# Optimization experiments

Measured on AMD Instinct MI355X. Metric: run time of the kernel, lower is better.

The kernel has to match this reference:

```python
import jax, jax.numpy as jnp
import numpy as np

T = 262144
S_IN, A_IN, S_OUT, G_OUT, H = 64, 16, 32, 16, 32


def setup_inputs() -> dict:
    key = jax.random.key(0)
    ks = jax.random.split(key, 16)
    def lin_w(k, i, o):
        return (jax.random.normal(k, (i, o), jnp.float32) / np.sqrt(i)).astype(jnp.float32)
    return {
        's': jax.random.normal(ks[0], (1, T, S_IN), jnp.float32),
        'a': jax.random.uniform(ks[1], (1, T, A_IN), jnp.float32),  # BCE targets in [0,1]
        'u': jax.random.uniform(ks[2], (1, T, 1), jnp.float32),     # Bernoulli noise
        'W1': lin_w(ks[3], 2 * (S_IN + A_IN), H), 'b1': jnp.zeros((H,), jnp.float32),
        'W2': lin_w(ks[4], 2 * H, H),             'b2': jnp.zeros((H,), jnp.float32),
        'W3': lin_w(ks[5], 2 * H, S_OUT + G_OUT + 1), 'b3': jnp.zeros((S_OUT + G_OUT + 1,), jnp.float32),
        'Wp1': lin_w(ks[6], S_IN + G_OUT, H),     'bp1': jnp.zeros((H,), jnp.float32),
        'Wp2': lin_w(ks[7], H, A_IN),             'bp2': jnp.zeros((A_IN,), jnp.float32),
    }


def gnn_layer(x, W, b):
    # GraphNetLayer: each node sees its own feature + global mean over the trajectory
    agg = jnp.broadcast_to(jnp.mean(x, axis=1, keepdims=True), x.shape)
    return jnp.concatenate([x, agg], axis=-1) @ W + b


def reference(s, a, u, W1, b1, W2, b2, W3, b3, Wp1, bp1, Wp2, bp2):
    # encode: GNN over [N,T,s_in+a_in]
    x = jnp.concatenate([s, a], axis=-1)
    h = jnp.tanh(gnn_layer(x, W1, b1))
    h = jnp.tanh(gnn_layer(h, W2, b2))
    out = gnn_layer(h, W3, b3)
    z, g, alpha_logit = jnp.split(out, [S_OUT, S_OUT + G_OUT], axis=-1)
    alpha = jax.nn.sigmoid(alpha_logit)

    # Bernoulli sample with externalized noise; no gradient through the sample
    hard_alpha = jax.lax.stop_gradient((u < alpha).astype(alpha.dtype))  # [1,T,1]
    log_probs = hard_alpha * jax.nn.log_sigmoid(alpha_logit) + (1.0 - hard_alpha) * jax.nn.log_sigmoid(-alpha_logit)
    reinforce_lp = jnp.mean(log_probs)

    # extend_goals_hard: carry last goal where alpha fired (N==1), ragged scan
    def step(prev, ga):
        gt, at = ga  # [G_OUT], [1]
        cur = jnp.where(at > 0, gt, prev)
        return cur, cur
    _, hard_g = jax.lax.scan(step, jnp.zeros((G_OUT,), g.dtype), (g[0], hard_alpha[0]))
    hard_g = hard_g[None]  # [1,T,G_OUT]

    # decode: goal-conditioned policy MLP
    logits = jnp.tanh(jnp.concatenate([s, hard_g], axis=-1) @ Wp1 + bp1) @ Wp2 + bp2

    # BCEWithLogits recon loss (use_prior=False, train_dynamics/correspondence=False)
    recon = -(a * jax.nn.log_sigmoid(logits) + (1.0 - a) * jax.nn.log_sigmoid(-logits))
    per_ts = recon
    loss = jnp.mean(per_ts) + reinforce_lp * jnp.mean(jax.lax.stop_gradient(per_ts))

    # padded equivalents of short_z/short_g (ragged gather z[0,mask]) returned as masked tensors
    return loss, logits, hard_alpha, hard_g
```

## Files before the change

### kernel.cpp

```cpp
#include <hip/hip_runtime.h>
#include <math.h>


#define TT 262144
#define NBT 1024
#define NBR 512

__device__ __forceinline__ float spf32(float x) {
  return fmaxf(x, 0.f) + log1pf(expf(-fabsf(x)));
}

__device__ __forceinline__ double exp64(double x) {
  const double LOG2E  = 1.4426950408889634074;
  const double LN2_HI = 6.93147180369123816490e-01;
  const double LN2_LO = 1.90821492927058770002e-10;
  double kd = rint(x * LOG2E);
  double r  = fma(-kd, LN2_HI, x);
  r = fma(-kd, LN2_LO, r);
  double p = 2.08767569878681e-9;
  p = fma(p, r, 2.505210838544172e-8);
  p = fma(p, r, 2.755731922398589e-7);
  p = fma(p, r, 2.7557319223985893e-6);
  p = fma(p, r, 2.48015873015873e-5);
  p = fma(p, r, 1.984126984126984e-4);
  p = fma(p, r, 1.388888888888889e-3);
  p = fma(p, r, 8.333333333333333e-3);
  p = fma(p, r, 4.1666666666666664e-2);
  p = fma(p, r, 1.6666666666666666e-1);
  p = fma(p, r, 0.5);
  p = fma(p, r, 1.0);
  p = fma(p, r, 1.0);
  int k = (int)kd;
  long long sb = ((long long)(k + 1023)) << 52;
  return p * __longlong_as_double(sb);
}

__device__ __forceinline__ double tanh64(double x) {
  double ax = fmin(fabs(x), 19.0);
  double e = exp64(2.0 * ax);
  double t = 1.0 - 2.0 / (e + 1.0);
  return x >= 0.0 ? t : -t;
}

template <int C>
__global__ __launch_bounds__(256) void reduce_cols(const float* __restrict__ in,
                                                   double* __restrict__ part) {
  const int rpb = 256 / C;
  int col = threadIdx.x & (C - 1);
  int sub = threadIdx.x / C;
  long row0 = (long)blockIdx.x * rpb + sub;
  long stride = (long)NBR * rpb;
  double acc = 0.0;
  for (long r = row0; r < TT; r += stride) acc += (double)in[r * C + col];
  __shared__ double sm[256];
  sm[threadIdx.x] = acc;
  __syncthreads();
  if (threadIdx.x < C) {
    double s = 0.0;
#pragma unroll
    for (int i = 0; i < rpb; ++i) s += sm[i * C + threadIdx.x];
    part[(long)blockIdx.x * C + threadIdx.x] = s;
  }
}

__global__ __launch_bounds__(640) void prep1(const double* __restrict__ ps_s,
                                             const double* __restrict__ ps_a,
                                             const float* __restrict__ W1,
                                             const float* __restrict__ b1,
                                             double invT, double* __restrict__ c1) {
  __shared__ double partial[80][8];
  __shared__ double mx[80];
  int tid = threadIdx.x;
  int col = tid >> 3, sub = tid & 7;
  double ssum = 0.0;
  if (col < 64) {
#pragma unroll
    for (int i = 0; i < 64; ++i) ssum += ps_s[(sub * 64 + i) * 64 + col];
  } else {
    int c = col - 64;
#pragma unroll
    for (int i = 0; i < 64; ++i) ssum += ps_a[(sub * 64 + i) * 16 + c];
  }
  partial[col][sub] = ssum;
  __syncthreads();
  if (tid < 80) {
    double s = 0.0;
#pragma unroll
    for (int i = 0; i < 8; ++i) s += partial[tid][i];
    mx[tid] = s * invT;
  }
  __syncthreads();
  if (tid < 32) {
    double acc = (double)b1[tid];
    for (int j = 0; j < 80; ++j) acc += mx[j] * (double)W1[(80 + j) * 32 + tid];
    c1[tid] = acc;
  }
}

__global__ __launch_bounds__(256) void prep2(const double* __restrict__ ps,
                                             const float* __restrict__ W2,
                                             const float* __restrict__ b2,
                                             double invT, double* __restrict__ c2) {
  __shared__ double partial[32][8];
  __shared__ double mh[32];
  int tid = threadIdx.x;
  int col = tid >> 3, sub = tid & 7;
  double ssum = 0.0;
#pragma unroll
  for (int i = 0; i < 128; ++i) ssum += ps[(sub * 128 + i) * 32 + col];
  partial[col][sub] = ssum;
  __syncthreads();
  if (tid < 32) {
    double s = 0.0;
#pragma unroll
    for (int i = 0; i < 8; ++i) s += partial[tid][i];
    mh[tid] = s * invT;
  }
  __syncthreads();
  if (tid < 32) {
    double acc = (double)b2[tid];
    for (int j = 0; j < 32; ++j) acc += mh[j] * (double)W2[(32 + j) * 32 + tid];
    c2[tid] = acc;
  }
}

__global__ __launch_bounds__(256) void prep3(const double* __restrict__ ps,
                                             const float* __restrict__ W3,
                                             const float* __restrict__ b3,
                                             double invT, double* __restrict__ c3) {
  __shared__ double partial[32][8];
  __shared__ double mh[32];
  int tid = threadIdx.x;
  int col = tid >> 3, sub = tid & 7;
  double ssum = 0.0;
#pragma unroll
  for (int i = 0; i < 128; ++i) ssum += ps[(sub * 128 + i) * 32 + col];
  partial[col][sub] = ssum;
  __syncthreads();
  if (tid < 32) {
    double s = 0.0;
#pragma unroll
    for (int i = 0; i < 8; ++i) s += partial[tid][i];
    mh[tid] = s * invT;
  }
  __syncthreads();
  if (tid < 17) {
    double acc = (double)b3[32 + tid];
    for (int j = 0; j < 32; ++j) acc += mh[j] * (double)W3[(32 + j) * 49 + 32 + tid];
    c3[tid] = acc;
  }
}


__global__ __launch_bounds__(256, 4) void h1_kernel(const float* __restrict__ s,
                                                    const float* __restrict__ a,
                                                    const float* __restrict__ W1,
                                                    const double* __restrict__ c1,
                                                    double* __restrict__ h,
                                                    double* __restrict__ ps_h) {
  __shared__ float Wl[80 * 32];
  __shared__ double ws[4 * 32];
  for (int i = threadIdx.x; i < 80 * 32; i += 256) Wl[i] = W1[i];
  __syncthreads();
  long t = (long)blockIdx.x * 256 + threadIdx.x;
  double acc[32];
#pragma unroll
  for (int k = 0; k < 32; ++k) acc[k] = c1[k];
  const float4* s4 = (const float4*)(s + t * 64);
#pragma unroll 2
  for (int q = 0; q < 16; ++q) {
    float4 v = s4[q];
    const float* w = &Wl[(q * 4) * 32];
    double x0 = (double)v.x, x1 = (double)v.y, x2 = (double)v.z, x3 = (double)v.w;
#pragma unroll
    for (int k = 0; k < 32; ++k)
      acc[k] += x0 * (double)w[k] + x1 * (double)w[32 + k] +
                x2 * (double)w[64 + k] + x3 * (double)w[96 + k];
  }
  const float4* a4 = (const float4*)(a + t * 16);
#pragma unroll 2
  for (int q = 0; q < 4; ++q) {
    float4 v = a4[q];
    const float* w = &Wl[(64 + q * 4) * 32];
    double x0 = (double)v.x, x1 = (double)v.y, x2 = (double)v.z, x3 = (double)v.w;
#pragma unroll
    for (int k = 0; k < 32; ++k)
      acc[k] += x0 * (double)w[k] + x1 * (double)w[32 + k] +
                x2 * (double)w[64 + k] + x3 * (double)w[96 + k];
  }
  double* o = h + (size_t)blockIdx.x * 8192 + threadIdx.x;
#pragma unroll
  for (int k = 0; k < 32; ++k) { acc[k] = tanh64(acc[k]); o[k * 256] = acc[k]; }
  int lane = threadIdx.x & 63, wave = threadIdx.x >> 6;
#pragma unroll
  for (int k = 0; k < 32; ++k) {
    double v = acc[k];
    v += __shfl_down(v, 32, 64); v += __shfl_down(v, 16, 64);
    v += __shfl_down(v, 8, 64);  v += __shfl_down(v, 4, 64);
    v += __shfl_down(v, 2, 64);  v += __shfl_down(v, 1, 64);
    if (lane == 0) ws[wave * 32 + k] = v;
  }
  __syncthreads();
  if (threadIdx.x < 32) {
    double ssum = ws[threadIdx.x] + ws[32 + threadIdx.x] + ws[64 + threadIdx.x] +
                  ws[96 + threadIdx.x];
    ps_h[blockIdx.x * 32 + threadIdx.x] = ssum;
  }
}

__global__ __launch_bounds__(256, 4) void h2_kernel(const double* __restrict__ hin,
                                                    const float* __restrict__ W2,
                                                    const double* __restrict__ c2,
                                                    double* __restrict__ hout,
                                                    double* __restrict__ ps_h) {
  __shared__ float Wl[32 * 32];
  __shared__ double ws[4 * 32];
  for (int i = threadIdx.x; i < 32 * 32; i += 256) Wl[i] = W2[i];
  __syncthreads();
  const double* x = hin + (size_t)blockIdx.x * 8192 + threadIdx.x;
  double acc[32];
#pragma unroll
  for (int k = 0; k < 32; ++k) acc[k] = c2[k];
#pragma unroll 4
  for (int j = 0; j < 32; ++j) {
    double xj = x[j * 256];
#pragma unroll
    for (int k = 0; k < 32; ++k) acc[k] += xj * (double)Wl[j * 32 + k];
  }
  double* o = hout + (size_t)blockIdx.x * 8192 + threadIdx.x;
#pragma unroll
  for (int k = 0; k < 32; ++k) { acc[k] = tanh64(acc[k]); o[k * 256] = acc[k]; }
  int lane = threadIdx.x & 63, wave = threadIdx.x >> 6;
#pragma unroll
  for (int k = 0; k < 32; ++k) {
    double v = acc[k];
    v += __shfl_down(v, 32, 64); v += __shfl_down(v, 16, 64);
    v += __shfl_down(v, 8, 64);  v += __shfl_down(v, 4, 64);
    v += __shfl_down(v, 2, 64);  v += __shfl_down(v, 1, 64);
    if (lane == 0) ws[wave * 32 + k] = v;
  }
  __syncthreads();
  if (threadIdx.x < 32) {
    double ssum = ws[threadIdx.x] + ws[32 + threadIdx.x] + ws[64 + threadIdx.x] +
                  ws[96 + threadIdx.x];
    ps_h[blockIdx.x * 32 + threadIdx.x] = ssum;
  }
}

__global__ __launch_bounds__(256, 4) void out_kernel(const double* __restrict__ h,
                                                     const float* __restrict__ W3,
                                                     const double* __restrict__ c3,
                                                     const float* __restrict__ u,
                                                     float* __restrict__ g, float* __restrict__ ha,
                                                     int* __restrict__ lastf,
                                                     double* __restrict__ lp_part) {
  __shared__ float Wl[32 * 17];
  __shared__ double sm[256];
  __shared__ unsigned long long wm[4];
  for (int i = threadIdx.x; i < 32 * 17; i += 256) {
    int j = i / 17, k = i - j * 17;
    Wl[i] = W3[j * 49 + 32 + k];
  }
  __syncthreads();
  long t = (long)blockIdx.x * 256 + threadIdx.x;
  const double* x = h + (size_t)blockIdx.x * 8192 + threadIdx.x;
  double acc[17];
#pragma unroll
  for (int k = 0; k < 17; ++k) acc[k] = c3[k];
#pragma unroll 4
  for (int j = 0; j < 32; ++j) {
    double xj = x[j * 256];
#pragma unroll
    for (int k = 0; k < 17; ++k) acc[k] += xj * (double)Wl[j * 17 + k];
  }
  float4* g4 = (float4*)(g + t * 16);
  float4 o0, o1, o2, o3;
  o0.x = (float)acc[0];  o0.y = (float)acc[1];  o0.z = (float)acc[2];  o0.w = (float)acc[3];
  o1.x = (float)acc[4];  o1.y = (float)acc[5];  o1.z = (float)acc[6];  o1.w = (float)acc[7];
  o2.x = (float)acc[8];  o2.y = (float)acc[9];  o2.z = (float)acc[10]; o2.w = (float)acc[11];
  o3.x = (float)acc[12]; o3.y = (float)acc[13]; o3.z = (float)acc[14]; o3.w = (float)acc[15];
  g4[0] = o0; g4[1] = o1; g4[2] = o2; g4[3] = o3;
  double l = acc[16];
  double lc = fmin(fmax(l, -700.0), 700.0);
  double alpha = 1.0 / (1.0 + exp64(-lc));
  bool fired = ((double)u[t]) < alpha;
  ha[t] = fired ? 1.f : 0.f;
  float lf = (float)l;
  sm[threadIdx.x] = (double)(fired ? -spf32(-lf) : -spf32(lf));
  unsigned long long bm = __ballot(fired ? 1 : 0);
  if ((threadIdx.x & 63) == 0) wm[threadIdx.x >> 6] = bm;
  __syncthreads();
  for (int off = 128; off > 0; off >>= 1) {
    if (threadIdx.x < off) sm[threadIdx.x] += sm[threadIdx.x + off];
    __syncthreads();
  }
  if (threadIdx.x == 0) {
    lp_part[blockIdx.x] = sm[0];
    int last = -1;
#pragma unroll
    for (int w = 3; w >= 0; --w) {
      if (last < 0 && wm[w])
        last = (int)((long)blockIdx.x * 256 + w * 64 + (63 - __builtin_clzll(wm[w])));
    }
    lastf[blockIdx.x] = last;
  }
}

__global__ __launch_bounds__(1024) void carry_scan(const int* __restrict__ lastf,
                                                   int* __restrict__ carry, int n) {
  __shared__ int sm[1024];
  int tid = threadIdx.x;
  sm[tid] = (tid < n) ? lastf[tid] : -1;
  __syncthreads();
  for (int off = 1; off < n; off <<= 1) {
    int v = sm[tid];
    int o = (tid >= off) ? sm[tid - off] : -1;
    __syncthreads();
    sm[tid] = v > o ? v : o;
    __syncthreads();
  }
  if (tid < n) carry[tid] = (tid == 0) ? -1 : sm[tid - 1];
}

__global__ __launch_bounds__(256, 2) void decode_kernel(
    const float* __restrict__ s, const float* __restrict__ a, const float* __restrict__ g,
    const float* __restrict__ Wp1, const float* __restrict__ bp1, const float* __restrict__ Wp2,
    const float* __restrict__ bp2, const float* __restrict__ ha, const int* __restrict__ carry,
    float* __restrict__ logits, float* __restrict__ hardg, double* __restrict__ rc_part) {
  __shared__ float W1l[80 * 32];
  __shared__ float W2l[32 * 16];
  __shared__ int wlast[4];
  __shared__ double sm[256];
  long t = (long)blockIdx.x * 256 + threadIdx.x;
  bool fired = ha[t] > 0.5f;
  unsigned long long m = __ballot(fired ? 1 : 0);
  int wave = threadIdx.x >> 6, lane = threadIdx.x & 63;
  if (lane == 0)
    wlast[wave] = m ? (int)((long)blockIdx.x * 256 + wave * 64 + (63 - __builtin_clzll(m))) : -1;
  for (int i = threadIdx.x; i < 80 * 32; i += 256) W1l[i] = Wp1[i];
  for (int i = threadIdx.x; i < 32 * 16; i += 256) W2l[i] = Wp2[i];
  __syncthreads();
  unsigned long long pm = m & (~0ULL >> (63 - lane));
  int idx = pm ? (int)((long)blockIdx.x * 256 + wave * 64 + (63 - __builtin_clzll(pm))) : -1;
#pragma unroll
  for (int w = 0; w < 4; ++w)
    if (w < wave && wlast[w] > idx) idx = wlast[w];
  int cr = carry[blockIdx.x];
  if (cr > idx) idx = cr;
  float msk = idx >= 0 ? 1.f : 0.f;
  const float4* g4 = (const float4*)(g + (long)(idx >= 0 ? idx : 0) * 16);
  float4 v0 = g4[0], v1 = g4[1], v2 = g4[2], v3 = g4[3];
  float hg0  = msk * v0.x, hg1  = msk * v0.y, hg2  = msk * v0.z, hg3  = msk * v0.w;
  float hg4  = msk * v1.x, hg5  = msk * v1.y, hg6  = msk * v1.z, hg7  = msk * v1.w;
  float hg8  = msk * v2.x, hg9  = msk * v2.y, hg10 = msk * v2.z, hg11 = msk * v2.w;
  float hg12 = msk * v3.x, hg13 = msk * v3.y, hg14 = msk * v3.z, hg15 = msk * v3.w;
  hardg[t * 16 + 0]  = hg0;  hardg[t * 16 + 1]  = hg1;
  hardg[t * 16 + 2]  = hg2;  hardg[t * 16 + 3]  = hg3;
  hardg[t * 16 + 4]  = hg4;  hardg[t * 16 + 5]  = hg5;
  hardg[t * 16 + 6]  = hg6;  hardg[t * 16 + 7]  = hg7;
  hardg[t * 16 + 8]  = hg8;  hardg[t * 16 + 9]  = hg9;
  hardg[t * 16 + 10] = hg10; hardg[t * 16 + 11] = hg11;
  hardg[t * 16 + 12] = hg12; hardg[t * 16 + 13] = hg13;
  hardg[t * 16 + 14] = hg14; hardg[t * 16 + 15] = hg15;
  float acc[32];
#pragma unroll
  for (int k = 0; k < 32; ++k) {
    float v = bp1[k];
    v += hg0  * W1l[(64 + 0)  * 32 + k];  v += hg1  * W1l[(64 + 1)  * 32 + k];
    v += hg2  * W1l[(64 + 2)  * 32 + k];  v += hg3  * W1l[(64 + 3)  * 32 + k];
    v += hg4  * W1l[(64 + 4)  * 32 + k];  v += hg5  * W1l[(64 + 5)  * 32 + k];
    v += hg6  * W1l[(64 + 6)  * 32 + k];  v += hg7  * W1l[(64 + 7)  * 32 + k];
    v += hg8  * W1l[(64 + 8)  * 32 + k];  v += hg9  * W1l[(64 + 9)  * 32 + k];
    v += hg10 * W1l[(64 + 10) * 32 + k];  v += hg11 * W1l[(64 + 11) * 32 + k];
    v += hg12 * W1l[(64 + 12) * 32 + k];  v += hg13 * W1l[(64 + 13) * 32 + k];
    v += hg14 * W1l[(64 + 14) * 32 + k];  v += hg15 * W1l[(64 + 15) * 32 + k];
    acc[k] = v;
  }
  const float4* s4 = (const float4*)(s + t * 64);
#pragma unroll 4
  for (int q = 0; q < 16; ++q) {
    float4 v = s4[q];
    const float* w = &W1l[(q * 4) * 32];
#pragma unroll
    for (int k = 0; k < 32; ++k)
      acc[k] += v.x * w[k] + v.y * w[32 + k] + v.z * w[64 + k] + v.w * w[96 + k];
  }
#pragma unroll
  for (int k = 0; k < 32; ++k) acc[k] = tanhf(acc[k]);
  float lg[16];
#pragma unroll
  for (int k = 0; k < 16; ++k) lg[k] = bp2[k];
#pragma unroll
  for (int j = 0; j < 32; ++j) {
    float hj = acc[j];
    const float* w = &W2l[j * 16];
#pragma unroll
    for (int k = 0; k < 16; ++k) lg[k] += hj * w[k];
  }
#pragma unroll
  for (int k = 0; k < 16; ++k) logits[t * 16 + k] = lg[k];
  const float4* a4 = (const float4*)(a + t * 16);
  double rs = 0.0;
#pragma unroll
  for (int q = 0; q < 4; ++q) {
    float4 av = a4[q];
    float l0 = lg[q * 4], l1 = lg[q * 4 + 1], l2 = lg[q * 4 + 2], l3 = lg[q * 4 + 3];
    rs += (double)(av.x * spf32(-l0) + (1.f - av.x) * spf32(l0));
    rs += (double)(av.y * spf32(-l1) + (1.f - av.y) * spf32(l1));
    rs += (double)(av.z * spf32(-l2) + (1.f - av.z) * spf32(l2));
    rs += (double)(av.w * spf32(-l3) + (1.f - av.w) * spf32(l3));
  }
  sm[threadIdx.x] = rs;
  __syncthreads();
  for (int off = 128; off > 0; off >>= 1) {
    if (threadIdx.x < off) sm[threadIdx.x] += sm[threadIdx.x + off];
    __syncthreads();
  }
  if (threadIdx.x == 0) rc_part[blockIdx.x] = sm[0];
}

__global__ __launch_bounds__(256) void finalize(const double* __restrict__ lp_part,
                                                const double* __restrict__ rc_part, int nb,
                                                double invT, float* __restrict__ out0) {
  __shared__ double s1[256], s2[256];
  int tid = threadIdx.x;
  double a1 = 0, a2 = 0;
  for (int i = tid; i < nb; i += 256) { a1 += lp_part[i]; a2 += rc_part[i]; }
  s1[tid] = a1; s2[tid] = a2;
  __syncthreads();
  for (int off = 128; off > 0; off >>= 1) {
    if (tid < off) { s1[tid] += s1[tid + off]; s2[tid] += s2[tid + off]; }
    __syncthreads();
  }
  if (tid == 0) {
    double R = s1[0] * invT;
    double M = s2[0] * invT / 16.0;
    out0[0] = (float)(M + R * M);
  }
}

extern "C" void kernel_launch(void* const* d_in, const int* in_sizes, int n_in,
                              void* d_out, int out_size, void* d_ws, size_t ws_size,
                              hipStream_t stream) {
  const float* s   = (const float*)d_in[0];
  const float* a   = (const float*)d_in[1];
  const float* u   = (const float*)d_in[2];
  const float* W1  = (const float*)d_in[3];
  const float* b1  = (const float*)d_in[4];
  const float* W2  = (const float*)d_in[5];
  const float* b2  = (const float*)d_in[6];
  const float* W3  = (const float*)d_in[7];
  const float* b3  = (const float*)d_in[8];
  const float* Wp1 = (const float*)d_in[9];
  const float* bp1 = (const float*)d_in[10];
  const float* Wp2 = (const float*)d_in[11];
  const float* bp2 = (const float*)d_in[12];

  const double invT = 1.0 / (double)TT;

  double* h      = (double*)d_ws;
  double* ps_s   = h + (size_t)TT * 32;
  double* ps_a   = ps_s + (size_t)NBR * 64;
  double* ps_h   = ps_a + (size_t)NBR * 16;
  double* c1     = ps_h + (size_t)NBT * 32;
  double* c2     = c1 + 32;
  double* c3     = c2 + 32;
  double* lp_part= c3 + 24;
  double* rc_part= lp_part + NBT;
  float*  g      = (float*)(rc_part + NBT);
  int*    lastf  = (int*)(g + (size_t)TT * 16);
  int*    carry  = lastf + NBT;

  float* out    = (float*)d_out;
  float* loss   = out;
  float* logits = out + 1;
  float* ha     = out + 1 + (size_t)TT * 16;
  float* hg     = ha + TT;

  reduce_cols<64><<<NBR, 256, 0, stream>>>(s, ps_s);
  reduce_cols<16><<<NBR, 256, 0, stream>>>(a, ps_a);
  prep1<<<1, 640, 0, stream>>>(ps_s, ps_a, W1, b1, invT, c1);
  h1_kernel<<<NBT, 256, 0, stream>>>(s, a, W1, c1, h, ps_h);
  prep2<<<1, 256, 0, stream>>>(ps_h, W2, b2, invT, c2);
  h2_kernel<<<NBT, 256, 0, stream>>>(h, W2, c2, h, ps_h);
  prep3<<<1, 256, 0, stream>>>(ps_h, W3, b3, invT, c3);
  out_kernel<<<NBT, 256, 0, stream>>>(h, W3, c3, u, g, ha, lastf, lp_part);
  carry_scan<<<1, NBT, 0, stream>>>(lastf, carry, NBT);
  decode_kernel<<<NBT, 256, 0, stream>>>(s, a, g, Wp1, bp1, Wp2, bp2, ha, carry,
                                         logits, hg, rc_part);
  finalize<<<1, 256, 0, stream>>>(lp_part, rc_part, NBT, invT, loss);
}
```

Before: 320.0 us.

## Run encoder in fp32 and recompute near-threshold Bernoulli decisions in fp64

The three encoder GNN layers now use fp32 arithmetic and fp32 intermediate storage instead of fp64, which halves the h buffer traffic and avoids slow double-precision FMAs. The Bernoulli decision is taken by comparing the logit with logit(u). Rows whose margin is below a small threshold go into a list that a new fixup kernel recomputes fully in fp64, so the discrete hard_alpha stays consistent with the double-precision reference. Loss partials and last-fire detection move into a separate stats kernel, which adds two launches and an atomic counter. The list is capped at a fixed size, so correctness depends on few rows landing near the threshold and on the margin covering the fp32 error.

```diff
diff --git a/kernel.cpp b/kernel.cpp
--- a/kernel.cpp
+++ b/kernel.cpp
@@ -5,6 +5,8 @@
 #define TT 262144
 #define NBT 1024
 #define NBR 512
+#define MARGIN 2e-3f
+#define LCAP 16384
 
 __device__ __forceinline__ float spf32(float x) {
   return fmaxf(x, 0.f) + log1pf(expf(-fabsf(x)));
@@ -152,49 +154,45 @@
 }
 
 
-__global__ __launch_bounds__(256, 4) void h1_kernel(const float* __restrict__ s,
-                                                    const float* __restrict__ a,
-                                                    const float* __restrict__ W1,
-                                                    const double* __restrict__ c1,
-                                                    double* __restrict__ h,
-                                                    double* __restrict__ ps_h) {
+__global__ __launch_bounds__(256, 4) void h1f(const float* __restrict__ s,
+                                              const float* __restrict__ a,
+                                              const float* __restrict__ W1,
+                                              const double* __restrict__ c1,
+                                              float* __restrict__ h,
+                                              double* __restrict__ ps_h) {
   __shared__ float Wl[80 * 32];
   __shared__ double ws[4 * 32];
   for (int i = threadIdx.x; i < 80 * 32; i += 256) Wl[i] = W1[i];
   __syncthreads();
   long t = (long)blockIdx.x * 256 + threadIdx.x;
-  double acc[32];
-#pragma unroll
-  for (int k = 0; k < 32; ++k) acc[k] = c1[k];
+  float acc[32];
+#pragma unroll
+  for (int k = 0; k < 32; ++k) acc[k] = (float)c1[k];
   const float4* s4 = (const float4*)(s + t * 64);
 #pragma unroll 2
   for (int q = 0; q < 16; ++q) {
     float4 v = s4[q];
     const float* w = &Wl[(q * 4) * 32];
-    double x0 = (double)v.x, x1 = (double)v.y, x2 = (double)v.z, x3 = (double)v.w;
 #pragma unroll
     for (int k = 0; k < 32; ++k)
-      acc[k] += x0 * (double)w[k] + x1 * (double)w[32 + k] +
-                x2 * (double)w[64 + k] + x3 * (double)w[96 + k];
+      acc[k] += v.x * w[k] + v.y * w[32 + k] + v.z * w[64 + k] + v.w * w[96 + k];
   }
   const float4* a4 = (const float4*)(a + t * 16);
 #pragma unroll 2
   for (int q = 0; q < 4; ++q) {
     float4 v = a4[q];
     const float* w = &Wl[(64 + q * 4) * 32];
-    double x0 = (double)v.x, x1 = (double)v.y, x2 = (double)v.z, x3 = (double)v.w;
 #pragma unroll
     for (int k = 0; k < 32; ++k)
-      acc[k] += x0 * (double)w[k] + x1 * (double)w[32 + k] +
-                x2 * (double)w[64 + k] + x3 * (double)w[96 + k];
-  }
-  double* o = h + (size_t)blockIdx.x * 8192 + threadIdx.x;
-#pragma unroll
-  for (int k = 0; k < 32; ++k) { acc[k] = tanh64(acc[k]); o[k * 256] = acc[k]; }
+      acc[k] += v.x * w[k] + v.y * w[32 + k] + v.z * w[64 + k] + v.w * w[96 + k];
+  }
+  float* o = h + (size_t)blockIdx.x * 8192 + threadIdx.x;
+#pragma unroll
+  for (int k = 0; k < 32; ++k) { acc[k] = tanhf(acc[k]); o[k * 256] = acc[k]; }
   int lane = threadIdx.x & 63, wave = threadIdx.x >> 6;
 #pragma unroll
   for (int k = 0; k < 32; ++k) {
-    double v = acc[k];
+    double v = (double)acc[k];
     v += __shfl_down(v, 32, 64); v += __shfl_down(v, 16, 64);
     v += __shfl_down(v, 8, 64);  v += __shfl_down(v, 4, 64);
     v += __shfl_down(v, 2, 64);  v += __shfl_down(v, 1, 64);
@@ -208,32 +206,32 @@
   }
 }
 
-__global__ __launch_bounds__(256, 4) void h2_kernel(const double* __restrict__ hin,
-                                                    const float* __restrict__ W2,
-                                                    const double* __restrict__ c2,
-                                                    double* __restrict__ hout,
-                                                    double* __restrict__ ps_h) {
+__global__ __launch_bounds__(256, 4) void h2f(const float* __restrict__ hin,
+                                              const float* __restrict__ W2,
+                                              const double* __restrict__ c2,
+                                              float* __restrict__ hout,
+                                              double* __restrict__ ps_h) {
   __shared__ float Wl[32 * 32];
   __shared__ double ws[4 * 32];
   for (int i = threadIdx.x; i < 32 * 32; i += 256) Wl[i] = W2[i];
   __syncthreads();
-  const double* x = hin + (size_t)blockIdx.x * 8192 + threadIdx.x;
-  double acc[32];
-#pragma unroll
-  for (int k = 0; k < 32; ++k) acc[k] = c2[k];
+  const float* x = hin + (size_t)blockIdx.x * 8192 + threadIdx.x;
+  float acc[32];
+#pragma unroll
+  for (int k = 0; k < 32; ++k) acc[k] = (float)c2[k];
 #pragma unroll 4
   for (int j = 0; j < 32; ++j) {
-    double xj = x[j * 256];
-#pragma unroll
-    for (int k = 0; k < 32; ++k) acc[k] += xj * (double)Wl[j * 32 + k];
-  }
-  double* o = hout + (size_t)blockIdx.x * 8192 + threadIdx.x;
-#pragma unroll
-  for (int k = 0; k < 32; ++k) { acc[k] = tanh64(acc[k]); o[k * 256] = acc[k]; }
+    float xj = x[j * 256];
+#pragma unroll
+    for (int k = 0; k < 32; ++k) acc[k] += xj * Wl[j * 32 + k];
+  }
+  float* o = hout + (size_t)blockIdx.x * 8192 + threadIdx.x;
+#pragma unroll
+  for (int k = 0; k < 32; ++k) { acc[k] = tanhf(acc[k]); o[k * 256] = acc[k]; }
   int lane = threadIdx.x & 63, wave = threadIdx.x >> 6;
 #pragma unroll
   for (int k = 0; k < 32; ++k) {
-    double v = acc[k];
+    double v = (double)acc[k];
     v += __shfl_down(v, 32, 64); v += __shfl_down(v, 16, 64);
     v += __shfl_down(v, 8, 64);  v += __shfl_down(v, 4, 64);
     v += __shfl_down(v, 2, 64);  v += __shfl_down(v, 1, 64);
@@ -247,45 +245,113 @@
   }
 }
 
-__global__ __launch_bounds__(256, 4) void out_kernel(const double* __restrict__ h,
-                                                     const float* __restrict__ W3,
-                                                     const double* __restrict__ c3,
-                                                     const float* __restrict__ u,
-                                                     float* __restrict__ g, float* __restrict__ ha,
-                                                     int* __restrict__ lastf,
-                                                     double* __restrict__ lp_part) {
+__global__ __launch_bounds__(256, 4) void outf(const float* __restrict__ h,
+                                               const float* __restrict__ W3,
+                                               const double* __restrict__ c3,
+                                               const float* __restrict__ u,
+                                               float* __restrict__ g,
+                                               float* __restrict__ lvals,
+                                               float* __restrict__ ha,
+                                               int* __restrict__ cnt,
+                                               int* __restrict__ list) {
   __shared__ float Wl[32 * 17];
-  __shared__ double sm[256];
-  __shared__ unsigned long long wm[4];
   for (int i = threadIdx.x; i < 32 * 17; i += 256) {
     int j = i / 17, k = i - j * 17;
     Wl[i] = W3[j * 49 + 32 + k];
   }
   __syncthreads();
   long t = (long)blockIdx.x * 256 + threadIdx.x;
-  const double* x = h + (size_t)blockIdx.x * 8192 + threadIdx.x;
-  double acc[17];
-#pragma unroll
-  for (int k = 0; k < 17; ++k) acc[k] = c3[k];
+  const float* x = h + (size_t)blockIdx.x * 8192 + threadIdx.x;
+  float acc[17];
+#pragma unroll
+  for (int k = 0; k < 17; ++k) acc[k] = (float)c3[k];
 #pragma unroll 4
   for (int j = 0; j < 32; ++j) {
-    double xj = x[j * 256];
-#pragma unroll
-    for (int k = 0; k < 17; ++k) acc[k] += xj * (double)Wl[j * 17 + k];
+    float xj = x[j * 256];
+#pragma unroll
+    for (int k = 0; k < 17; ++k) acc[k] += xj * Wl[j * 17 + k];
   }
   float4* g4 = (float4*)(g + t * 16);
   float4 o0, o1, o2, o3;
-  o0.x = (float)acc[0];  o0.y = (float)acc[1];  o0.z = (float)acc[2];  o0.w = (float)acc[3];
-  o1.x = (float)acc[4];  o1.y = (float)acc[5];  o1.z = (float)acc[6];  o1.w = (float)acc[7];
-  o2.x = (float)acc[8];  o2.y = (float)acc[9];  o2.z = (float)acc[10]; o2.w = (float)acc[11];
-  o3.x = (float)acc[12]; o3.y = (float)acc[13]; o3.z = (float)acc[14]; o3.w = (float)acc[15];
+  o0.x = acc[0];  o0.y = acc[1];  o0.z = acc[2];  o0.w = acc[3];
+  o1.x = acc[4];  o1.y = acc[5];  o1.z = acc[6];  o1.w = acc[7];
+  o2.x = acc[8];  o2.y = acc[9];  o2.z = acc[10]; o2.w = acc[11];
+  o3.x = acc[12]; o3.y = acc[13]; o3.z = acc[14]; o3.w = acc[15];
   g4[0] = o0; g4[1] = o1; g4[2] = o2; g4[3] = o3;
-  double l = acc[16];
-  double lc = fmin(fmax(l, -700.0), 700.0);
-  double alpha = 1.0 / (1.0 + exp64(-lc));
-  bool fired = ((double)u[t]) < alpha;
-  ha[t] = fired ? 1.f : 0.f;
-  float lf = (float)l;
+  float l = acc[16];
+  lvals[t] = l;
+  float uu = u[t];
+  float lu = (uu <= 0.f) ? -1e30f : (logf(uu) - logf(1.f - uu));
+  float d = l - lu;
+  ha[t] = (d > 0.f) ? 1.f : 0.f;
+  if (fabsf(d) < MARGIN) {
+    int i = atomicAdd(cnt, 1);
+    if (i < LCAP) list[i] = (int)t;
+  }
+}
+
+__global__ __launch_bounds__(64, 2) void fixk(const float* __restrict__ s,
+                                              const float* __restrict__ a,
+                                              const float* __restrict__ u,
+                                              const float* __restrict__ W1,
+                                              const float* __restrict__ W2,
+                                              const float* __restrict__ W3,
+                                              const double* __restrict__ c1,
+                                              const double* __restrict__ c2,
+                                              const double* __restrict__ c3,
+                                              const int* __restrict__ cnt,
+                                              const int* __restrict__ list,
+                                              float* __restrict__ ha) {
+  int n = *cnt;
+  if (n > LCAP) n = LCAP;
+  for (int i = blockIdx.x * 64 + threadIdx.x; i < n; i += gridDim.x * 64) {
+    int row = list[i];
+    double a1[32];
+#pragma unroll
+    for (int k = 0; k < 32; ++k) a1[k] = c1[k];
+#pragma unroll 4
+    for (int j = 0; j < 64; ++j) {
+      double xj = (double)s[(size_t)row * 64 + j];
+#pragma unroll
+      for (int k = 0; k < 32; ++k) a1[k] += xj * (double)W1[j * 32 + k];
+    }
+#pragma unroll 4
+    for (int j = 0; j < 16; ++j) {
+      double xj = (double)a[(size_t)row * 16 + j];
+#pragma unroll
+      for (int k = 0; k < 32; ++k) a1[k] += xj * (double)W1[(64 + j) * 32 + k];
+    }
+#pragma unroll
+    for (int k = 0; k < 32; ++k) a1[k] = tanh64(a1[k]);
+    double a2[32];
+#pragma unroll
+    for (int k = 0; k < 32; ++k) a2[k] = c2[k];
+#pragma unroll
+    for (int j = 0; j < 32; ++j) {
+      double xj = a1[j];
+#pragma unroll
+      for (int k = 0; k < 32; ++k) a2[k] += xj * (double)W2[j * 32 + k];
+    }
+#pragma unroll
+    for (int k = 0; k < 32; ++k) a2[k] = tanh64(a2[k]);
+    double l = c3[16];
+#pragma unroll
+    for (int j = 0; j < 32; ++j) l += a2[j] * (double)W3[j * 49 + 48];
+    double lc = fmin(fmax(l, -700.0), 700.0);
+    double alpha = 1.0 / (1.0 + exp64(-lc));
+    ha[row] = (((double)u[row]) < alpha) ? 1.f : 0.f;
+  }
+}
+
+__global__ __launch_bounds__(256, 4) void statsk(const float* __restrict__ ha,
+                                                 const float* __restrict__ lvals,
+                                                 int* __restrict__ lastf,
+                                                 double* __restrict__ lp_part) {
+  __shared__ double sm[256];
+  __shared__ unsigned long long wm[4];
+  long t = (long)blockIdx.x * 256 + threadIdx.x;
+  bool fired = ha[t] > 0.5f;
+  float lf = lvals[t];
   sm[threadIdx.x] = (double)(fired ? -spf32(-lf) : -spf32(lf));
   unsigned long long bm = __ballot(fired ? 1 : 0);
   if ((threadIdx.x & 63) == 0) wm[threadIdx.x >> 6] = bm;
@@ -458,18 +524,21 @@
 
   const double invT = 1.0 / (double)TT;
 
-  double* h      = (double*)d_ws;
-  double* ps_s   = h + (size_t)TT * 32;
+  double* ps_s   = (double*)d_ws;
   double* ps_a   = ps_s + (size_t)NBR * 64;
   double* ps_h   = ps_a + (size_t)NBR * 16;
   double* c1     = ps_h + (size_t)NBT * 32;
   double* c2     = c1 + 32;
   double* c3     = c2 + 32;
-  double* lp_part= c3 + 24;
-  double* rc_part= lp_part + NBT;
-  float*  g      = (float*)(rc_part + NBT);
-  int*    lastf  = (int*)(g + (size_t)TT * 16);
+  double* lp     = c3 + 24;
+  double* rc     = lp + NBT;
+  float*  g      = (float*)(rc + NBT);
+  float*  h      = g + (size_t)TT * 16;
+  float*  lvals  = h + (size_t)TT * 32;
+  int*    lastf  = (int*)(lvals + TT);
   int*    carry  = lastf + NBT;
+  int*    cnt    = carry + NBT;
+  int*    list   = cnt + 4;
 
   float* out    = (float*)d_out;
   float* loss   = out;
@@ -477,16 +546,19 @@
   float* ha     = out + 1 + (size_t)TT * 16;
   float* hg     = ha + TT;
 
+  hipMemsetAsync((void*)cnt, 0, sizeof(int), stream);
   reduce_cols<64><<<NBR, 256, 0, stream>>>(s, ps_s);
   reduce_cols<16><<<NBR, 256, 0, stream>>>(a, ps_a);
   prep1<<<1, 640, 0, stream>>>(ps_s, ps_a, W1, b1, invT, c1);
-  h1_kernel<<<NBT, 256, 0, stream>>>(s, a, W1, c1, h, ps_h);
+  h1f<<<NBT, 256, 0, stream>>>(s, a, W1, c1, h, ps_h);
   prep2<<<1, 256, 0, stream>>>(ps_h, W2, b2, invT, c2);
-  h2_kernel<<<NBT, 256, 0, stream>>>(h, W2, c2, h, ps_h);
+  h2f<<<NBT, 256, 0, stream>>>(h, W2, c2, h, ps_h);
   prep3<<<1, 256, 0, stream>>>(ps_h, W3, b3, invT, c3);
-  out_kernel<<<NBT, 256, 0, stream>>>(h, W3, c3, u, g, ha, lastf, lp_part);
+  outf<<<NBT, 256, 0, stream>>>(h, W3, c3, u, g, lvals, ha, cnt, list);
+  fixk<<<32, 64, 0, stream>>>(s, a, u, W1, W2, W3, c1, c2, c3, cnt, list, ha);
+  statsk<<<NBT, 256, 0, stream>>>(ha, lvals, lastf, lp);
   carry_scan<<<1, NBT, 0, stream>>>(lastf, carry, NBT);
   decode_kernel<<<NBT, 256, 0, stream>>>(s, a, g, Wp1, bp1, Wp2, bp2, ha, carry,
-                                         logits, hg, rc_part);
-  finalize<<<1, 256, 0, stream>>>(lp_part, rc_part, NBT, invT, loss);
-}
+                                         logits, hg, rc);
+  finalize<<<1, 256, 0, stream>>>(lp, rc, NBT, invT, loss);
+}
```

Result: slower. 612.5 us (+91.4%).
